# Kernel optimization log

Hardware: AMD Instinct MI355X
Metric: run time of the kernel (lower is better)

Reference implementation:

```python
import jax, jax.numpy as jnp
import numpy as np

D_MODEL = 1024
NUM_HEADS = 8
D_K = D_MODEL // NUM_HEADS
NEG_INF = -1e9
EPS = 1e-6


def setup_inputs() -> dict:
    key = jax.random.key(0)
    ks = jax.random.split(key, 10)
    B, S = 4, 2048
    scale = 1.0 / np.sqrt(D_MODEL)
    return {
        "queries": jax.random.normal(ks[0], (B, S, D_MODEL), jnp.float32),
        "keys": jax.random.normal(ks[1], (B, S, D_MODEL), jnp.float32),
        "values": jax.random.normal(ks[2], (B, S, D_MODEL), jnp.float32),
        "Wq": jax.random.normal(ks[3], (D_MODEL, D_MODEL), jnp.float32) * scale,
        "bq": jnp.zeros((D_MODEL,), jnp.float32),
        "Wk": jax.random.normal(ks[4], (D_MODEL, D_MODEL), jnp.float32) * scale,
        "bk": jnp.zeros((D_MODEL,), jnp.float32),
        "Wv": jax.random.normal(ks[5], (D_MODEL, D_MODEL), jnp.float32) * scale,
        "bv": jnp.zeros((D_MODEL,), jnp.float32),
        "gamma": jnp.ones((D_MODEL,), jnp.float32),
        "beta": jnp.zeros((D_MODEL,), jnp.float32),
    }


def _split_heads(x, B, S):
    # [B,S,D] -> [B,H,S,d_k]
    return x.reshape(B, S, NUM_HEADS, D_K).transpose(0, 2, 1, 3)


def reference(queries, keys, values, Wq, bq, Wk, bk, Wv, bv, gamma, beta):
    B, S, _ = queries.shape
    Q = _split_heads(queries @ Wq + bq, B, S)
    K = _split_heads(keys @ Wk + bk, B, keys.shape[1])
    V = _split_heads(values @ Wv + bv, B, values.shape[1])
    scores = jnp.einsum("bhqd,bhkd->bhqk", Q, K) / jnp.sqrt(jnp.float32(D_K))
    # causal mask (lower triangular kept)
    Sk = scores.shape[-1]
    mask = jnp.tril(jnp.ones((scores.shape[-2], Sk), dtype=bool))
    scores = jnp.where(mask, scores, jnp.float32(NEG_INF))
    attn = jax.nn.softmax(scores, axis=-1)
    # dropout disabled (training=False)
    out = jnp.einsum("bhqk,bhkd->bhqd", attn, V)
    out = out.transpose(0, 2, 1, 3).reshape(B, S, D_MODEL)
    resid = out + queries
    mu = jnp.mean(resid, axis=-1, keepdims=True)
    var = jnp.var(resid, axis=-1, keepdims=True)
    normed = (resid - mu) / jnp.sqrt(var + EPS)
    return normed * gamma + beta
```

## Files before the change

kernel.cpp:

```cpp
#include <hip/hip_runtime.h>
#include <hip/hip_bf16.h>
#include <stdint.h>

#define D_MODEL 1024
#define S_LEN   2048
#define BATCH   4
#define NH      8
#define DK      128

typedef __attribute__((ext_vector_type(8))) __bf16 bf16x8;
typedef __attribute__((ext_vector_type(4))) float  f32x4;

__device__ __forceinline__ f32x4 mfma16(bf16x8 a, bf16x8 b, f32x4 c) {
  return __builtin_amdgcn_mfma_f32_16x16x32_bf16(a, b, c, 0, 0, 0);
}

__device__ __forceinline__ void gld_lds16(const void* g, void* l) {
  __builtin_amdgcn_global_load_lds(
      (const __attribute__((address_space(1))) void*)g,
      (__attribute__((address_space(3))) void*)l, 16, 0, 0);
}

#define ATTN_SCALE 0.08838834764831845f

__global__ __launch_bounds__(256) void cvt_kernel(
    const float* __restrict__ x0, const float* __restrict__ x1,
    const float* __restrict__ x2, __hip_bfloat16* __restrict__ out) {
  const size_t N = (size_t)BATCH * S_LEN * D_MODEL;
  const int w = blockIdx.y;
  const float* src = (w == 0) ? x0 : (w == 1) ? x1 : x2;
  __hip_bfloat16* dst = out + (size_t)w * N;
  const size_t i = ((size_t)blockIdx.x * 256 + threadIdx.x) * 4;
  const float4 v = *(const float4*)(src + i);
  *(__hip_bfloat162*)(dst + i)     = __float22bfloat162_rn(make_float2(v.x, v.y));
  *(__hip_bfloat162*)(dst + i + 2) = __float22bfloat162_rn(make_float2(v.z, v.w));
}

__global__ void wtrans_kernel(const float* __restrict__ Wq,
                              const float* __restrict__ Wk,
                              const float* __restrict__ Wv,
                              __hip_bfloat16* __restrict__ Wt) {
  __shared__ __hip_bfloat16 tile[32][33];
  const int w = blockIdx.z;
  const float* src = (w == 0) ? Wq : (w == 1) ? Wk : Wv;
  const float sc = (w == 0) ? ATTN_SCALE : 1.0f;
  __hip_bfloat16* dst = Wt + (size_t)w * D_MODEL * D_MODEL;
  const int tx = threadIdx.x, ty = threadIdx.y;
  int x = blockIdx.x * 32 + tx;
  int y = blockIdx.y * 32 + ty;
  for (int i = 0; i < 32; i += 8)
    tile[ty + i][tx] = __float2bfloat16(src[(size_t)(y + i) * D_MODEL + x] * sc);
  __syncthreads();
  x = blockIdx.y * 32 + tx;
  y = blockIdx.x * 32 + ty;
  for (int i = 0; i < 32; i += 8)
    dst[(size_t)(y + i) * D_MODEL + x] = tile[tx][ty + i];
}

__global__ __launch_bounds__(256) void qkv_gemm_kernel(
    const __hip_bfloat16* __restrict__ Xbf,
    const float* __restrict__ bq, const float* __restrict__ bk,
    const float* __restrict__ bv,
    const __hip_bfloat16* __restrict__ Wt,
    __hip_bfloat16* __restrict__ Qo, __hip_bfloat16* __restrict__ Ko,
    __hip_bfloat16* __restrict__ Vo) {
  const int flat = blockIdx.x;
  const int xcd  = flat & 7;
  const int idx  = flat >> 3;
  const int n_t  = idx & 7;
  const int mg   = idx >> 3;
  const int pair = xcd * 24 + mg;
  const int which = pair >> 6;
  const int m_t   = pair & 63;

  const size_t N = (size_t)BATCH * S_LEN * D_MODEL;
  const __hip_bfloat16* X = Xbf + (size_t)which * N;
  const __hip_bfloat16* W = Wt + (size_t)which * D_MODEL * D_MODEL;
  const float* bias = (which == 0) ? bq : (which == 1) ? bk : bv;
  const float bscale = (which == 0) ? ATTN_SCALE : 1.0f;

  __shared__ __align__(16) __hip_bfloat16 Asm[128 * 32];
  __shared__ __align__(16) __hip_bfloat16 Bsm[128 * 32];

  const int tid  = threadIdx.x;
  const int lane = tid & 63;
  const int wv   = tid >> 6;
  const int lo16 = lane & 15;
  const int hi4  = lane >> 4;
  const int m0 = m_t * 128;
  const int n0 = n_t * 128;
  const int wm = (wv >> 1) * 64;
  const int wn = (wv & 1) * 64;

  f32x4 acc[4][4];
  const f32x4 z4 = {0.f, 0.f, 0.f, 0.f};
  for (int i = 0; i < 4; ++i)
    for (int j = 0; j < 4; ++j) acc[i][j] = z4;

  for (int k0 = 0; k0 < D_MODEL; k0 += 32) {
    __syncthreads();
    for (int it = 0; it < 2; ++it) {
      const int cbase = it * 256 + wv * 64;
      const int c = cbase + lane;
      gld_lds16(X + (size_t)(m0 + (c >> 2)) * D_MODEL + k0 + (c & 3) * 8,
                &Asm[cbase * 8]);
      gld_lds16(W + (size_t)(n0 + (c >> 2)) * D_MODEL + k0 + (c & 3) * 8,
                &Bsm[cbase * 8]);
    }
    __syncthreads();

    bf16x8 af[4], bfr[4];
    for (int i = 0; i < 4; ++i)
      af[i] = *(const bf16x8*)&Asm[(wm + 16 * i + lo16) * 32 + hi4 * 8];
    for (int j = 0; j < 4; ++j)
      bfr[j] = *(const bf16x8*)&Bsm[(wn + 16 * j + lo16) * 32 + hi4 * 8];
    for (int i = 0; i < 4; ++i)
      for (int j = 0; j < 4; ++j)
        acc[i][j] = mfma16(af[i], bfr[j], acc[i][j]);
  }

  const int b = m0 >> 11;
  for (int j = 0; j < 4; ++j) {
    const int n = n0 + wn + j * 16 + lo16;
    const float bval = bias[n] * bscale;
    const int h = n >> 7;
    const int d = n & 127;
    for (int i = 0; i < 4; ++i) {
      for (int r = 0; r < 4; ++r) {
        const int m = m0 + wm + 16 * i + hi4 * 4 + r;
        const int s = m & (S_LEN - 1);
        const __hip_bfloat16 ob = __float2bfloat16(acc[i][j][r] + bval);
        if (which == 0)
          Qo[((size_t)(b * NH + h) * S_LEN + s) * DK + d] = ob;
        else if (which == 1)
          Ko[((size_t)(b * NH + h) * S_LEN + s) * DK + d] = ob;
        else
          Vo[((size_t)(b * NH + h) * DK + d) * S_LEN + s] = ob;
      }
    }
  }
}

__global__ __launch_bounds__(256) void attn_kernel(
    const __hip_bfloat16* __restrict__ Qw, const __hip_bfloat16* __restrict__ Kw,
    const __hip_bfloat16* __restrict__ Vtw, __hip_bfloat16* __restrict__ Og) {
  const int t = 15 - blockIdx.x;
  const int h = blockIdx.y;
  const int b = blockIdx.z;
  const int tid  = threadIdx.x;
  const int lane = tid & 63;
  const int wv   = tid >> 6;
  const int lo16 = lane & 15;
  const int hi4  = lane >> 4;

  const int qrow0  = t * 128 + wv * 32;
  const int ns_w   = 4 * t + wv + 1;
  const int nsteps = 4 * t + 4;

  const size_t bh = (size_t)(b * NH + h);
  const __hip_bfloat16* Qp = Qw + bh * S_LEN * DK;
  const __hip_bfloat16* Kp = Kw + bh * S_LEN * DK;
  const __hip_bfloat16* Vp = Vtw + bh * DK * S_LEN;

  __shared__ __align__(16) __hip_bfloat16 Ksm[3][32 * 128];
  __shared__ __align__(16) __hip_bfloat16 Vsm[3][128 * 32];
  __shared__ __align__(16) __hip_bfloat16 Psm[4][32 * 40];

  bf16x8 qf[2][4];
  for (int m = 0; m < 2; ++m)
    for (int kk = 0; kk < 4; ++kk)
      qf[m][kk] = *(const bf16x8*)&Qp[(size_t)(qrow0 + m * 16 + lo16) * DK +
                                      kk * 32 + hi4 * 8];

  f32x4 oacc[2][8];
  const f32x4 z4 = {0.f, 0.f, 0.f, 0.f};
  for (int m = 0; m < 2; ++m)
    for (int j = 0; j < 8; ++j) oacc[m][j] = z4;
  float lsum[2][4];
  for (int m = 0; m < 2; ++m)
    for (int i = 0; i < 4; ++i) lsum[m][i] = 0.f;

  auto stage = [&](int st, int buf) {
    const int kv0 = st << 5;
    for (int it = 0; it < 2; ++it) {
      const int cbase = it * 256 + wv * 64;
      const int c = cbase + lane;
      gld_lds16(Kp + (size_t)(kv0 + (c & 31)) * DK + (c >> 5) * 8,
                &Ksm[buf][cbase * 8]);
      gld_lds16(Vp + (size_t)(c & 127) * S_LEN + kv0 + (c >> 7) * 8,
                &Vsm[buf][cbase * 8]);
    }
  };

  stage(0, 0);
  stage(1, 1);

  int bsel = 0;
  for (int st = 0; st < nsteps; ++st) {
    if (st + 1 < nsteps)
      asm volatile("s_waitcnt vmcnt(4)" ::: "memory");
    else
      asm volatile("s_waitcnt vmcnt(0)" ::: "memory");
    __builtin_amdgcn_s_barrier();
    asm volatile("" ::: "memory");

    if (st < ns_w) {
      const __hip_bfloat16* Kb = Ksm[bsel];
      const __hip_bfloat16* Vb = Vsm[bsel];

      bf16x8 kf[2][4];
      for (int kn = 0; kn < 2; ++kn)
        for (int kk = 0; kk < 4; ++kk)
          kf[kn][kk] = *(const bf16x8*)&Kb[((kk * 4 + hi4) * 32 + kn * 16 + lo16) * 8];
      f32x4 sc[2][2];
      for (int m = 0; m < 2; ++m)
        for (int kn = 0; kn < 2; ++kn) {
          f32x4 s4 = z4;
          for (int kk = 0; kk < 4; ++kk)
            s4 = mfma16(qf[m][kk], kf[kn][kk], s4);
          sc[m][kn] = s4;
        }

      const int kv0 = st << 5;
      const bool do_mask = (st == ns_w - 1);
      for (int m = 0; m < 2; ++m) {
        for (int i = 0; i < 4; ++i) {
          const int qg = qrow0 + m * 16 + hi4 * 4 + i;
          float s0 = sc[m][0][i];
          float s1 = sc[m][1][i];
          if (do_mask) {
            if (kv0 + lo16 > qg)      s0 = -1.0e30f;
            if (kv0 + 16 + lo16 > qg) s1 = -1.0e30f;
          }
          const float p0 = __expf(s0 - 8.f);
          const float p1 = __expf(s1 - 8.f);
          lsum[m][i] += p0 + p1;
          const int prw = m * 16 + hi4 * 4 + i;
          Psm[wv][prw * 40 + lo16]      = __float2bfloat16(p0);
          Psm[wv][prw * 40 + 16 + lo16] = __float2bfloat16(p1);
        }
      }
      asm volatile("s_waitcnt lgkmcnt(0)" ::: "memory");

      bf16x8 pf[2];
      for (int m = 0; m < 2; ++m)
        pf[m] = *(const bf16x8*)&Psm[wv][(m * 16 + lo16) * 40 + hi4 * 8];
      for (int j = 0; j < 8; ++j) {
        const bf16x8 vf = *(const bf16x8*)&Vb[(hi4 * 128 + j * 16 + lo16) * 8];
        oacc[0][j] = mfma16(pf[0], vf, oacc[0][j]);
        oacc[1][j] = mfma16(pf[1], vf, oacc[1][j]);
      }
    }

    if (st + 2 < nsteps) {
      int nb = bsel + 2; if (nb >= 3) nb -= 3;
      stage(st + 2, nb);
    }
    if (++bsel == 3) bsel = 0;
  }

  for (int m = 0; m < 2; ++m) {
    for (int i = 0; i < 4; ++i) {
      float l = lsum[m][i];
      l += __shfl_xor(l, 1);
      l += __shfl_xor(l, 2);
      l += __shfl_xor(l, 4);
      l += __shfl_xor(l, 8);
      const float inv = 1.0f / l;
      const int qg = qrow0 + m * 16 + hi4 * 4 + i;
      __hip_bfloat16* orow = Og + ((size_t)b * S_LEN + qg) * D_MODEL + h * DK;
      for (int j = 0; j < 8; ++j)
        orow[j * 16 + lo16] = __float2bfloat16(oacc[m][j][i] * inv);
    }
  }
}

__global__ __launch_bounds__(256) void ln_kernel(
    const __hip_bfloat16* __restrict__ Og, const float* __restrict__ resid_in,
    const float* __restrict__ gamma, const float* __restrict__ beta,
    float* __restrict__ out) {
  const int row = blockIdx.x;
  const __hip_bfloat16* orow = Og + (size_t)row * D_MODEL;
  const float* qrow = resid_in + (size_t)row * D_MODEL;
  const int tid = threadIdx.x;
  const int base = tid * 4;
  const float4 q4 = *(const float4*)(qrow + base);
  const ushort4 o4 = *(const ushort4*)(orow + base);
  float v[4];
  v[0] = __bfloat162float(*(const __hip_bfloat16*)&o4.x) + q4.x;
  v[1] = __bfloat162float(*(const __hip_bfloat16*)&o4.y) + q4.y;
  v[2] = __bfloat162float(*(const __hip_bfloat16*)&o4.z) + q4.z;
  v[3] = __bfloat162float(*(const __hip_bfloat16*)&o4.w) + q4.w;
  float s = v[0] + v[1] + v[2] + v[3];
  float ss = v[0] * v[0] + v[1] * v[1] + v[2] * v[2] + v[3] * v[3];
  for (int m = 1; m < 64; m <<= 1) { s += __shfl_xor(s, m); ss += __shfl_xor(ss, m); }
  __shared__ float red[8];
  const int wv = tid >> 6, lane = tid & 63;
  if (lane == 0) { red[wv] = s; red[4 + wv] = ss; }
  __syncthreads();
  s  = red[0] + red[1] + red[2] + red[3];
  ss = red[4] + red[5] + red[6] + red[7];
  const float mu  = s * (1.0f / D_MODEL);
  const float var = ss * (1.0f / D_MODEL) - mu * mu;
  const float rstd = rsqrtf(var + 1e-6f);
  const float4 g4 = *(const float4*)(gamma + base);
  const float4 b4 = *(const float4*)(beta + base);
  float4 o;
  o.x = (v[0] - mu) * rstd * g4.x + b4.x;
  o.y = (v[1] - mu) * rstd * g4.y + b4.y;
  o.z = (v[2] - mu) * rstd * g4.z + b4.z;
  o.w = (v[3] - mu) * rstd * g4.w + b4.w;
  *(float4*)(out + (size_t)row * D_MODEL + base) = o;
}

extern "C" void kernel_launch(void* const* d_in, const int* in_sizes, int n_in,
                              void* d_out, int out_size, void* d_ws, size_t ws_size,
                              hipStream_t stream) {
  const float* queries = (const float*)d_in[0];
  const float* keys    = (const float*)d_in[1];
  const float* values  = (const float*)d_in[2];
  const float* Wq = (const float*)d_in[3];
  const float* bq = (const float*)d_in[4];
  const float* Wk = (const float*)d_in[5];
  const float* bk = (const float*)d_in[6];
  const float* Wv = (const float*)d_in[7];
  const float* bv = (const float*)d_in[8];
  const float* gamma = (const float*)d_in[9];
  const float* beta  = (const float*)d_in[10];

  char* ws = (char*)d_ws;
  const size_t N = (size_t)BATCH * S_LEN * D_MODEL;
  const size_t WT_BYTES  = (size_t)3 * D_MODEL * D_MODEL * 2;
  const size_t XBF_BYTES = (size_t)3 * N * 2;
  const size_t QKV_BYTES = (size_t)BATCH * NH * S_LEN * DK * 2;
  __hip_bfloat16* Wt  = (__hip_bfloat16*)ws;
  __hip_bfloat16* Xbf = (__hip_bfloat16*)(ws + WT_BYTES);
  __hip_bfloat16* Ogs = (__hip_bfloat16*)(ws + WT_BYTES);
  __hip_bfloat16* Qws = (__hip_bfloat16*)(ws + WT_BYTES + XBF_BYTES);
  __hip_bfloat16* Kws = (__hip_bfloat16*)(ws + WT_BYTES + XBF_BYTES + QKV_BYTES);
  __hip_bfloat16* Vws = (__hip_bfloat16*)(ws + WT_BYTES + XBF_BYTES + 2 * QKV_BYTES);

  cvt_kernel<<<dim3((unsigned)(N / 1024), 3), 256, 0, stream>>>(queries, keys, values, Xbf);
  wtrans_kernel<<<dim3(32, 32, 3), dim3(32, 8), 0, stream>>>(Wq, Wk, Wv, Wt);
  qkv_gemm_kernel<<<dim3(1536), 256, 0, stream>>>(
      Xbf, bq, bk, bv, Wt, Qws, Kws, Vws);
  attn_kernel<<<dim3(16, NH, BATCH), 256, 0, stream>>>(Qws, Kws, Vws, Ogs);
  ln_kernel<<<dim3(BATCH * S_LEN), 256, 0, stream>>>(Ogs, queries, gamma, beta,
                                                     (float*)d_out);
}
```

Baseline: 387.5 us.

## Split long causal attention tiles across two blocks with balanced schedule table

The causal attention grid is reorganised into 768 blocks driven by a lookup table. Query tiles 8-15 have their key range split into two halves, each handled by its own block, and tiles 0-7 run whole, so per-block work is more even and the MI355X CUs stay busier. Split halves write unnormalised fp32 partial outputs and row sums to workspace, and the layernorm kernel merges and normalises them. The K/V staging pipeline also drops from triple to double buffering with precomputed base pointers and a full vmcnt(0) wait each step. This costs extra fp32 partial traffic, less prefetch depth, and workspace aliasing that depends on the buffer lifetimes (lsumP sits at the start of the workspace, over the converted weights).

```diff
diff --git a/kernel.cpp b/kernel.cpp
--- a/kernel.cpp
+++ b/kernel.cpp
@@ -141,29 +141,52 @@
   }
 }
 
+__device__ const uint32_t ATTN_TBL[24] = {
+  79, 95, 32,
+  78, 94, 33,
+  77, 93, 34,
+  76, 92, 35,
+  75, 91, 36,
+  39, 72, 88,
+  38, 73, 89,
+  37, 74, 90
+};
+
 __global__ __launch_bounds__(256) void attn_kernel(
     const __hip_bfloat16* __restrict__ Qw, const __hip_bfloat16* __restrict__ Kw,
-    const __hip_bfloat16* __restrict__ Vtw, __hip_bfloat16* __restrict__ Og) {
-  const int t = 15 - blockIdx.x;
-  const int h = blockIdx.y;
-  const int b = blockIdx.z;
+    const __hip_bfloat16* __restrict__ Vtw, __hip_bfloat16* __restrict__ Og,
+    float* __restrict__ partO, float* __restrict__ lsumP) {
+  const int bid = blockIdx.x;
+  const int q8  = bid & 255;
+  const int rr  = bid >> 8;
+  const int bh  = q8 & 31;
+  const int jrow = q8 >> 5;
+  const int h   = bh & 7;
+  const int b   = bh >> 3;
+  const uint32_t wi = ATTN_TBL[jrow * 3 + rr];
+  const int  t     = wi & 15;
+  const int  chnk  = (wi >> 4) & 1;
+  const bool split = (wi >> 5) == 2;
+  const int  half  = 2 * t + 2;
+  const int  st0   = (split && chnk == 1) ? half : 0;
+  const int  stN   = (split && chnk == 0) ? half : (4 * t + 4);
+
   const int tid  = threadIdx.x;
   const int lane = tid & 63;
   const int wv   = tid >> 6;
   const int lo16 = lane & 15;
   const int hi4  = lane >> 4;
 
-  const int qrow0  = t * 128 + wv * 32;
-  const int ns_w   = 4 * t + wv + 1;
-  const int nsteps = 4 * t + 4;
-
-  const size_t bh = (size_t)(b * NH + h);
-  const __hip_bfloat16* Qp = Qw + bh * S_LEN * DK;
-  const __hip_bfloat16* Kp = Kw + bh * S_LEN * DK;
-  const __hip_bfloat16* Vp = Vtw + bh * DK * S_LEN;
-
-  __shared__ __align__(16) __hip_bfloat16 Ksm[3][32 * 128];
-  __shared__ __align__(16) __hip_bfloat16 Vsm[3][128 * 32];
+  const int qrow0 = t * 128 + wv * 32;
+  const int ns_w  = 4 * t + wv + 1;
+
+  const size_t bhp = (size_t)(b * NH + h);
+  const __hip_bfloat16* Qp = Qw + bhp * S_LEN * DK;
+  const __hip_bfloat16* Kp = Kw + bhp * S_LEN * DK;
+  const __hip_bfloat16* Vp = Vtw + bhp * DK * S_LEN;
+
+  __shared__ __align__(16) __hip_bfloat16 Ksm[2][32 * 128];
+  __shared__ __align__(16) __hip_bfloat16 Vsm[2][128 * 32];
   __shared__ __align__(16) __hip_bfloat16 Psm[4][32 * 40];
 
   bf16x8 qf[2][4];
@@ -180,29 +203,31 @@
   for (int m = 0; m < 2; ++m)
     for (int i = 0; i < 4; ++i) lsum[m][i] = 0.f;
 
+  const __hip_bfloat16* kbase[2];
+  const __hip_bfloat16* vbase[2];
+#pragma unroll
+  for (int it = 0; it < 2; ++it) {
+    const int c = it * 256 + tid;
+    kbase[it] = Kp + (size_t)(c & 31) * DK + (c >> 5) * 8;
+    vbase[it] = Vp + (size_t)(c & 127) * S_LEN + (c >> 7) * 8;
+  }
   auto stage = [&](int st, int buf) {
-    const int kv0 = st << 5;
+#pragma unroll
     for (int it = 0; it < 2; ++it) {
-      const int cbase = it * 256 + wv * 64;
-      const int c = cbase + lane;
-      gld_lds16(Kp + (size_t)(kv0 + (c & 31)) * DK + (c >> 5) * 8,
-                &Ksm[buf][cbase * 8]);
-      gld_lds16(Vp + (size_t)(c & 127) * S_LEN + kv0 + (c >> 7) * 8,
-                &Vsm[buf][cbase * 8]);
+      const int cb = (it * 256 + wv * 64) * 8;
+      gld_lds16(kbase[it] + (st << 12), &Ksm[buf][cb]);
+      gld_lds16(vbase[it] + (st << 5),  &Vsm[buf][cb]);
     }
   };
 
-  stage(0, 0);
-  stage(1, 1);
+  stage(st0, 0);
 
   int bsel = 0;
-  for (int st = 0; st < nsteps; ++st) {
-    if (st + 1 < nsteps)
-      asm volatile("s_waitcnt vmcnt(4)" ::: "memory");
-    else
-      asm volatile("s_waitcnt vmcnt(0)" ::: "memory");
+  for (int st = st0; st < stN; ++st) {
+    asm volatile("s_waitcnt vmcnt(0)" ::: "memory");
     __builtin_amdgcn_s_barrier();
     asm volatile("" ::: "memory");
+    if (st + 1 < stN) stage(st + 1, bsel ^ 1);
 
     if (st < ns_w) {
       const __hip_bfloat16* Kb = Ksm[bsel];
@@ -251,12 +276,7 @@
         oacc[1][j] = mfma16(pf[1], vf, oacc[1][j]);
       }
     }
-
-    if (st + 2 < nsteps) {
-      int nb = bsel + 2; if (nb >= 3) nb -= 3;
-      stage(st + 2, nb);
-    }
-    if (++bsel == 3) bsel = 0;
+    bsel ^= 1;
   }
 
   for (int m = 0; m < 2; ++m) {
@@ -266,31 +286,61 @@
       l += __shfl_xor(l, 2);
       l += __shfl_xor(l, 4);
       l += __shfl_xor(l, 8);
-      const float inv = 1.0f / l;
-      const int qg = qrow0 + m * 16 + hi4 * 4 + i;
-      __hip_bfloat16* orow = Og + ((size_t)b * S_LEN + qg) * D_MODEL + h * DK;
-      for (int j = 0; j < 8; ++j)
-        orow[j * 16 + lo16] = __float2bfloat16(oacc[m][j][i] * inv);
+      const int row = wv * 32 + m * 16 + hi4 * 4 + i;
+      if (!split) {
+        const float inv = 1.0f / l;
+        const int qg = t * 128 + row;
+        __hip_bfloat16* orow = Og + ((size_t)b * S_LEN + qg) * D_MODEL + h * DK;
+        for (int j = 0; j < 8; ++j)
+          orow[j * 16 + lo16] = __float2bfloat16(oacc[m][j][i] * inv);
+      } else {
+        const int pidx = bh * 8 + (t - 8);
+        float* prow = partO +
+            (((size_t)chnk * 256 + pidx) * 128 + row) * 128;
+        for (int j = 0; j < 8; ++j)
+          prow[j * 16 + lo16] = oacc[m][j][i];
+        if (lo16 == 0)
+          lsumP[(chnk * 256 + pidx) * 128 + row] = l;
+      }
     }
   }
 }
 
 __global__ __launch_bounds__(256) void ln_kernel(
-    const __hip_bfloat16* __restrict__ Og, const float* __restrict__ resid_in,
+    const __hip_bfloat16* __restrict__ Og, const float* __restrict__ partO,
+    const float* __restrict__ lsumP, const float* __restrict__ resid_in,
     const float* __restrict__ gamma, const float* __restrict__ beta,
     float* __restrict__ out) {
-  const int row = blockIdx.x;
-  const __hip_bfloat16* orow = Og + (size_t)row * D_MODEL;
-  const float* qrow = resid_in + (size_t)row * D_MODEL;
-  const int tid = threadIdx.x;
+  const int row  = blockIdx.x;
+  const int b    = row >> 11;
+  const int srow = row & (S_LEN - 1);
+  const int tile = srow >> 7;
+  const int tid  = threadIdx.x;
   const int base = tid * 4;
-  const float4 q4 = *(const float4*)(qrow + base);
-  const ushort4 o4 = *(const ushort4*)(orow + base);
+  const float4 q4 = *(const float4*)(resid_in + (size_t)row * D_MODEL + base);
   float v[4];
-  v[0] = __bfloat162float(*(const __hip_bfloat16*)&o4.x) + q4.x;
-  v[1] = __bfloat162float(*(const __hip_bfloat16*)&o4.y) + q4.y;
-  v[2] = __bfloat162float(*(const __hip_bfloat16*)&o4.z) + q4.z;
-  v[3] = __bfloat162float(*(const __hip_bfloat16*)&o4.w) + q4.w;
+  if (tile < 8) {
+    const __hip_bfloat16* orow = Og + (size_t)row * D_MODEL;
+    const ushort4 o4 = *(const ushort4*)(orow + base);
+    v[0] = __bfloat162float(*(const __hip_bfloat16*)&o4.x) + q4.x;
+    v[1] = __bfloat162float(*(const __hip_bfloat16*)&o4.y) + q4.y;
+    v[2] = __bfloat162float(*(const __hip_bfloat16*)&o4.z) + q4.z;
+    v[3] = __bfloat162float(*(const __hip_bfloat16*)&o4.w) + q4.w;
+  } else {
+    const int h    = base >> 7;
+    const int rin  = srow & 127;
+    const int pidx = (b * 8 + h) * 8 + (tile - 8);
+    const size_t off = ((size_t)pidx * 128 + rin) * 128 + (base & 127);
+    const float4 p0 = *(const float4*)(partO + off);
+    const float4 p1 = *(const float4*)(partO + (size_t)256 * 128 * 128 + off);
+    const float l = lsumP[pidx * 128 + rin] +
+                    lsumP[256 * 128 + pidx * 128 + rin];
+    const float inv = 1.0f / l;
+    v[0] = (p0.x + p1.x) * inv + q4.x;
+    v[1] = (p0.y + p1.y) * inv + q4.y;
+    v[2] = (p0.z + p1.z) * inv + q4.z;
+    v[3] = (p0.w + p1.w) * inv + q4.w;
+  }
   float s = v[0] + v[1] + v[2] + v[3];
   float ss = v[0] * v[0] + v[1] * v[1] + v[2] * v[2] + v[3] * v[3];
   for (int m = 1; m < 64; m <<= 1) { s += __shfl_xor(s, m); ss += __shfl_xor(ss, m); }
@@ -333,9 +383,12 @@
   const size_t WT_BYTES  = (size_t)3 * D_MODEL * D_MODEL * 2;
   const size_t XBF_BYTES = (size_t)3 * N * 2;
   const size_t QKV_BYTES = (size_t)BATCH * NH * S_LEN * DK * 2;
+  const size_t OG_BYTES  = (size_t)BATCH * S_LEN * D_MODEL * 2;
   __hip_bfloat16* Wt  = (__hip_bfloat16*)ws;
   __hip_bfloat16* Xbf = (__hip_bfloat16*)(ws + WT_BYTES);
   __hip_bfloat16* Ogs = (__hip_bfloat16*)(ws + WT_BYTES);
+  float* partO = (float*)(ws + WT_BYTES + OG_BYTES);
+  float* lsumP = (float*)ws;
   __hip_bfloat16* Qws = (__hip_bfloat16*)(ws + WT_BYTES + XBF_BYTES);
   __hip_bfloat16* Kws = (__hip_bfloat16*)(ws + WT_BYTES + XBF_BYTES + QKV_BYTES);
   __hip_bfloat16* Vws = (__hip_bfloat16*)(ws + WT_BYTES + XBF_BYTES + 2 * QKV_BYTES);
@@ -344,7 +397,7 @@
   wtrans_kernel<<<dim3(32, 32, 3), dim3(32, 8), 0, stream>>>(Wq, Wk, Wv, Wt);
   qkv_gemm_kernel<<<dim3(1536), 256, 0, stream>>>(
       Xbf, bq, bk, bv, Wt, Qws, Kws, Vws);
-  attn_kernel<<<dim3(16, NH, BATCH), 256, 0, stream>>>(Qws, Kws, Vws, Ogs);
-  ln_kernel<<<dim3(BATCH * S_LEN), 256, 0, stream>>>(Ogs, queries, gamma, beta,
-                                                     (float*)d_out);
-}
+  attn_kernel<<<dim3(768), 256, 0, stream>>>(Qws, Kws, Vws, Ogs, partO, lsumP);
+  ln_kernel<<<dim3(BATCH * S_LEN), 256, 0, stream>>>(Ogs, partO, lsumP, queries,
+                                                     gamma, beta, (float*)d_out);
+}
```

New measurement: 370.5 us. 1.05x faster.
